# Kernel tuning notes

Measured on AMD Instinct MI355X. Metric: run time of the kernel, lower is better.

The kernel has to match this reference:

```python
import jax, jax.numpy as jnp
import numpy as np

DIM = 768
H = 12        # query heads
HKV = 4       # kv heads
G = H // HKV  # GQA group size
HD = 64       # head dim
CAP = 50.0    # soft cap (Gemma-2 style)
EPS = 1e-6
SCALE = HD ** -0.5
B, T, S = 1, 128, 256


def setup_inputs() -> dict:
    key = jax.random.key(0)
    ks = jax.random.split(key, 5)
    s = DIM ** -0.5
    x = jax.random.normal(ks[0], (B, T, S, DIM), jnp.float32)
    Wq = jax.random.normal(ks[1], (DIM, H * HD), jnp.float32) * s
    Wk = jax.random.normal(ks[2], (DIM, HKV * HD), jnp.float32) * s
    Wv = jax.random.normal(ks[3], (DIM, HKV * HD), jnp.float32) * s
    Wo = jax.random.normal(ks[4], (H * HD, DIM), jnp.float32) * s
    q_norm_w = jnp.ones((HD,), jnp.float32)
    k_norm_w = jnp.ones((HD,), jnp.float32)
    return {"x": x, "Wq": Wq, "Wk": Wk, "Wv": Wv, "Wo": Wo,
            "q_norm_w": q_norm_w, "k_norm_w": k_norm_w}


def _rmsnorm(x, w):
    # x: (..., HD)
    return x * jax.lax.rsqrt(jnp.mean(x * x, axis=-1, keepdims=True) + EPS) * w


def reference(x, Wq, Wk, Wv, Wo, q_norm_w, k_norm_w):
    b, t, s, d = x.shape
    n = b * s
    # fold spatial into batch: temporal attention per spatial position
    xf = x.transpose(0, 2, 1, 3).reshape(n, t, d)             # (N, T, D)
    q = (xf @ Wq).reshape(n, t, H, HD).transpose(0, 2, 1, 3)   # (N, H, T, hd)
    k = (xf @ Wk).reshape(n, t, HKV, HD).transpose(0, 2, 1, 3) # (N, Hkv, T, hd)
    v = (xf @ Wv).reshape(n, t, HKV, HD).transpose(0, 2, 1, 3)
    # QKNorm (per-head RMSNorm on head_dim)
    q = _rmsnorm(q, q_norm_w)
    k = _rmsnorm(k, k_norm_w)
    # GQA without materializing repeated K/V: split q heads into (Hkv, G)
    # (repeat_interleave maps query head h -> kv head h // G, matching kv*G+g)
    qg = q.reshape(n, HKV, G, t, HD)
    attn = jnp.einsum('bkgtd,bksd->bkgts', qg, k) * SCALE      # (N, Hkv, G, T, T)
    attn = CAP * jnp.tanh(attn / CAP)                          # soft cap
    causal = jnp.triu(jnp.ones((t, t), bool), 1)               # True above diag
    attn = jnp.where(causal, -jnp.inf, attn)
    attn = jax.nn.softmax(attn, axis=-1)
    out = jnp.einsum('bkgts,bksd->bkgtd', attn, v)             # (N, Hkv, G, T, hd)
    out = out.reshape(n, H, t, HD).transpose(0, 2, 1, 3).reshape(n, t, H * HD)
    out = out @ Wo                                             # (N, T, D)
    return out.reshape(b, s, t, d).transpose(0, 2, 1, 3)        # (B, T, S, D)
```

## Files before the change

### kernel.cpp

```cpp
#include <hip/hip_runtime.h>
#include <stdint.h>
#include <stddef.h>

#define DIM 768
#define NH  12
#define NKV 4
#define HD  64
#define TT  128
#define NS  256

typedef __attribute__((ext_vector_type(8))) short bf16x8;
typedef __attribute__((ext_vector_type(4))) float f32x4;
typedef __attribute__((ext_vector_type(4))) unsigned int u32x4;
typedef __attribute__((ext_vector_type(2))) unsigned int u32x2;

__device__ __forceinline__ unsigned short f2bf(float f) {
  union { float f; unsigned int u; } v; v.f = f;
  return (unsigned short)((v.u + 0x7FFFu + ((v.u >> 16) & 1u)) >> 16);
}

__global__ __launch_bounds__(256)
void prep_kernel(const float* __restrict__ x, const float* __restrict__ Wq,
                 const float* __restrict__ Wk, const float* __restrict__ Wv,
                 const float* __restrict__ Wo, unsigned short* __restrict__ Wt,
                 unsigned short* __restrict__ WoT, unsigned short* __restrict__ xb) {
  const int b = blockIdx.x, tid = threadIdx.x;
  if (b < 6144) {
    int idx = b * 256 + tid;
    const int n1 = 1280 * DIM;
    if (idx < n1) {
      int c = idx / DIM, kk = idx - c * DIM;
      float v;
      if (c < 768)       v = Wq[kk * 768 + c];
      else if (c < 1024) v = Wk[kk * 256 + (c - 768)];
      else               v = Wv[kk * 256 + (c - 1024)];
      Wt[idx] = f2bf(v);
    } else {
      int i2 = idx - n1;
      int c = i2 / DIM, kk = i2 - c * DIM;
      WoT[i2] = f2bf(Wo[kk * 768 + c]);
    }
  } else {
    int g = (b - 6144) * 256 + tid;
    int r = g / 192;
    int k = g - r * 192;
    int t = r >> 8, n = r & 255;
    f32x4 f = *reinterpret_cast<const f32x4*>(x + (size_t)g * 4);
    u32x2 pk;
    pk[0] = (unsigned)f2bf(f[0]) | ((unsigned)f2bf(f[1]) << 16);
    pk[1] = (unsigned)f2bf(f[2]) | ((unsigned)f2bf(f[3]) << 16);
    *reinterpret_cast<u32x2*>(xb + (size_t)((n << 7) + t) * DIM + k * 4) = pk;
  }
}

__global__ __launch_bounds__(256)
void qkv_kernel(const unsigned short* __restrict__ xb, const float* __restrict__ qnw,
                const float* __restrict__ knw, const unsigned short* __restrict__ Wt,
                unsigned short* __restrict__ qb, unsigned short* __restrict__ kb,
                unsigned short* __restrict__ vTb) {
  const int b = blockIdx.x;
  const int x8 = b & 7, ib = b >> 3;
  const int cb = ib % 10;
  const int n  = (ib / 10) * 8 + x8;
  const int tid = threadIdx.x;
  const int wave = tid >> 6, lane = tid & 63;
  const int cl = lane & 15, rowg = lane >> 4;
  const int wr = wave >> 1, wc = wave & 1;
  __shared__ unsigned short As[128][72];
  __shared__ unsigned short Bs[128][72];
  f32x4 acc[4][4] = {};
  const int col0 = cb * 128;
  for (int ko = 0; ko < DIM; ko += 64) {
    __syncthreads();
    #pragma unroll
    for (int i2 = 0; i2 < 4; ++i2) {
      int c = tid + 256 * i2, r = c >> 3, seg = c & 7;
      *reinterpret_cast<u32x4*>(&As[r][seg * 8]) =
          *reinterpret_cast<const u32x4*>(xb + (size_t)(n * TT + r) * DIM + ko + seg * 8);
    }
    #pragma unroll
    for (int i2 = 0; i2 < 4; ++i2) {
      int c = tid + 256 * i2, r = c >> 3, seg = c & 7;
      *reinterpret_cast<u32x4*>(&Bs[r][seg * 8]) =
          *reinterpret_cast<const u32x4*>(Wt + (size_t)(col0 + r) * DIM + ko + seg * 8);
    }
    __syncthreads();
    #pragma unroll
    for (int ks = 0; ks < 2; ++ks) {
      bf16x8 a[4], bb[4];
      #pragma unroll
      for (int m = 0; m < 4; ++m)
        a[m] = *reinterpret_cast<const bf16x8*>(&As[wr * 64 + m * 16 + cl][ks * 32 + rowg * 8]);
      #pragma unroll
      for (int nn = 0; nn < 4; ++nn)
        bb[nn] = *reinterpret_cast<const bf16x8*>(&Bs[wc * 64 + nn * 16 + cl][ks * 32 + rowg * 8]);
      #pragma unroll
      for (int m = 0; m < 4; ++m)
        #pragma unroll
        for (int nn = 0; nn < 4; ++nn)
          acc[m][nn] = __builtin_amdgcn_mfma_f32_16x16x32_bf16(a[m], bb[nn], acc[m][nn], 0, 0, 0);
    }
  }
  const int typ = (cb < 6) ? 0 : (cb < 8 ? 1 : 2);
  if (typ == 2) {
    const int kv = (cb - 8) * 2 + wc;
    unsigned short* dst = vTb + (size_t)((n * NKV + kv) * HD) * TT;
    #pragma unroll
    for (int m = 0; m < 4; ++m) {
      const int tb = wr * 64 + m * 16 + rowg * 4;
      #pragma unroll
      for (int nn = 0; nn < 4; ++nn) {
        const int d = nn * 16 + cl;
        u32x2 pk;
        pk[0] = (unsigned)f2bf(acc[m][nn][0]) | ((unsigned)f2bf(acc[m][nn][1]) << 16);
        pk[1] = (unsigned)f2bf(acc[m][nn][2]) | ((unsigned)f2bf(acc[m][nn][3]) << 16);
        *reinterpret_cast<u32x2*>(dst + (size_t)d * TT + tb) = pk;
      }
    }
  } else {
    const float* nw = (typ == 0) ? qnw : knw;
    float wfrag[4];
    #pragma unroll
    for (int nn = 0; nn < 4; ++nn) wfrag[nn] = nw[nn * 16 + cl];
    const float rs = (typ == 0) ? 0.125f : 1.0f;
    unsigned short* dst;
    if (typ == 0) { const int hh = cb * 2 + wc; dst = qb + (size_t)(n * NH + hh) * TT * HD; }
    else          { const int kv = (cb - 6) * 2 + wc; dst = kb + (size_t)(n * NKV + kv) * TT * HD; }
    #pragma unroll
    for (int m = 0; m < 4; ++m) {
      #pragma unroll
      for (int j = 0; j < 4; ++j) {
        const int t = wr * 64 + m * 16 + rowg * 4 + j;
        float ss = 0.f;
        #pragma unroll
        for (int nn = 0; nn < 4; ++nn) { float v = acc[m][nn][j]; ss += v * v; }
        #pragma unroll
        for (int dlt = 1; dlt < 16; dlt <<= 1) ss += __shfl_xor(ss, dlt);
        const float r = rsqrtf(ss * (1.f / 64.f) + 1e-6f) * rs;
        #pragma unroll
        for (int nn = 0; nn < 4; ++nn)
          dst[(size_t)t * HD + nn * 16 + cl] = f2bf(acc[m][nn][j] * r * wfrag[nn]);
      }
    }
  }
}

__global__ __launch_bounds__(256)
void attn_kernel(const unsigned short* __restrict__ qb, const unsigned short* __restrict__ kb,
                 const unsigned short* __restrict__ vTb, unsigned short* __restrict__ ab) {
  const int b = blockIdx.x;
  const int x8 = b & 7, ib = b >> 3;
  const int h = ib % 12;
  const int n = (ib / 12) * 8 + x8;
  const int kv = h / 3;
  const int tid = threadIdx.x, wave = tid >> 6, lane = tid & 63;
  const int cl = lane & 15, rowg = lane >> 4;
  __shared__ __align__(16) char smem[52224];
  unsigned short (*Qs)[72]  = reinterpret_cast<unsigned short (*)[72]>(smem);
  unsigned short (*Ks)[72]  = reinterpret_cast<unsigned short (*)[72]>(smem + 18432);
  unsigned short (*Pl)[136] = reinterpret_cast<unsigned short (*)[136]>(smem);
  unsigned short (*Vts)[136] = reinterpret_cast<unsigned short (*)[136]>(smem + 34816);

  const unsigned short* qsrc = qb + (size_t)(n * NH + h) * TT * HD;
  const unsigned short* ksrc = kb + (size_t)(n * NKV + kv) * TT * HD;
  #pragma unroll
  for (int i = 0; i < 4; ++i) {
    int c = tid + 256 * i, r = c >> 3, seg = c & 7;
    *reinterpret_cast<u32x4*>(&Qs[r][seg * 8]) = *reinterpret_cast<const u32x4*>(qsrc + c * 8);
  }
  #pragma unroll
  for (int i = 0; i < 4; ++i) {
    int c = tid + 256 * i, r = c >> 3, seg = c & 7;
    *reinterpret_cast<u32x4*>(&Ks[r][seg * 8]) = *reinterpret_cast<const u32x4*>(ksrc + c * 8);
  }
  __syncthreads();
  f32x4 sc[2][8] = {};
  #pragma unroll
  for (int ks = 0; ks < 2; ++ks) {
    bf16x8 a[2], bbf[8];
    #pragma unroll
    for (int m = 0; m < 2; ++m)
      a[m] = *reinterpret_cast<const bf16x8*>(&Qs[wave * 32 + m * 16 + cl][ks * 32 + rowg * 8]);
    #pragma unroll
    for (int nn = 0; nn < 8; ++nn)
      bbf[nn] = *reinterpret_cast<const bf16x8*>(&Ks[nn * 16 + cl][ks * 32 + rowg * 8]);
    #pragma unroll
    for (int m = 0; m < 2; ++m)
      #pragma unroll
      for (int nn = 0; nn < 8; ++nn)
        sc[m][nn] = __builtin_amdgcn_mfma_f32_16x16x32_bf16(a[m], bbf[nn], sc[m][nn], 0, 0, 0);
  }
  __syncthreads();
  const unsigned short* vsrc = vTb + (size_t)(n * NKV + kv) * HD * TT;
  #pragma unroll
  for (int i = 0; i < 4; ++i) {
    int c = tid + 256 * i, r = c >> 4, seg = c & 15;
    *reinterpret_cast<u32x4*>(&Vts[r][seg * 8]) = *reinterpret_cast<const u32x4*>(vsrc + c * 8);
  }
  #pragma unroll
  for (int m = 0; m < 2; ++m) {
    #pragma unroll
    for (int j = 0; j < 4; ++j) {
      const int rowv = wave * 32 + m * 16 + rowg * 4 + j;
      float mx = -__builtin_inff();
      #pragma unroll
      for (int nn = 0; nn < 8; ++nn) {
        float s = sc[m][nn][j];
        float e = __expf(s * 0.04f);
        s = 50.f - 100.f * __builtin_amdgcn_rcpf(e + 1.f);
        if (nn * 16 + cl > rowv) s = -__builtin_inff();
        sc[m][nn][j] = s;
        mx = fmaxf(mx, s);
      }
      #pragma unroll
      for (int d = 1; d < 16; d <<= 1) mx = fmaxf(mx, __shfl_xor(mx, d));
      float sum = 0.f;
      #pragma unroll
      for (int nn = 0; nn < 8; ++nn) {
        float e = __expf(sc[m][nn][j] - mx);
        sc[m][nn][j] = e;
        sum += e;
      }
      #pragma unroll
      for (int d = 1; d < 16; d <<= 1) sum += __shfl_xor(sum, d);
      const float inv = __builtin_amdgcn_rcpf(sum);
      #pragma unroll
      for (int nn = 0; nn < 8; ++nn)
        Pl[rowv][nn * 16 + cl] = f2bf(sc[m][nn][j] * inv);
    }
  }
  __syncthreads();
  f32x4 o[2][4] = {};
  #pragma unroll
  for (int ks = 0; ks < 4; ++ks) {
    bf16x8 a[2], bbf[4];
    #pragma unroll
    for (int m = 0; m < 2; ++m)
      a[m] = *reinterpret_cast<const bf16x8*>(&Pl[wave * 32 + m * 16 + cl][ks * 32 + rowg * 8]);
    #pragma unroll
    for (int nn = 0; nn < 4; ++nn)
      bbf[nn] = *reinterpret_cast<const bf16x8*>(&Vts[nn * 16 + cl][ks * 32 + rowg * 8]);
    #pragma unroll
    for (int m = 0; m < 2; ++m)
      #pragma unroll
      for (int nn = 0; nn < 4; ++nn)
        o[m][nn] = __builtin_amdgcn_mfma_f32_16x16x32_bf16(a[m], bbf[nn], o[m][nn], 0, 0, 0);
  }
  unsigned short* dst = ab + (size_t)n * TT * 768 + h * 64;
  #pragma unroll
  for (int m = 0; m < 2; ++m)
    #pragma unroll
    for (int j = 0; j < 4; ++j) {
      int t = wave * 32 + m * 16 + rowg * 4 + j;
      #pragma unroll
      for (int nn = 0; nn < 4; ++nn)
        dst[(size_t)t * 768 + nn * 16 + cl] = f2bf(o[m][nn][j]);
    }
}

__global__ __launch_bounds__(256)
void out_kernel(const unsigned short* __restrict__ ab, const unsigned short* __restrict__ WoT,
                float* __restrict__ out) {
  const int b = blockIdx.x;
  const int x8 = b & 7, ib = b >> 3;
  const int cb = ib % 6;
  const int n  = (ib / 6) * 8 + x8;
  const int tid = threadIdx.x, wave = tid >> 6, lane = tid & 63;
  const int cl = lane & 15, rowg = lane >> 4;
  const int wr = wave >> 1, wc = wave & 1;
  __shared__ unsigned short As[128][72];
  __shared__ unsigned short Bs[128][72];
  f32x4 acc[4][4] = {};
  for (int ko = 0; ko < DIM; ko += 64) {
    __syncthreads();
    #pragma unroll
    for (int i2 = 0; i2 < 4; ++i2) {
      int c = tid + 256 * i2, r = c >> 3, seg = c & 7;
      *reinterpret_cast<u32x4*>(&As[r][seg * 8]) =
          *reinterpret_cast<const u32x4*>(ab + (size_t)(n * TT + r) * DIM + ko + seg * 8);
    }
    #pragma unroll
    for (int i2 = 0; i2 < 4; ++i2) {
      int c = tid + 256 * i2, r = c >> 3, seg = c & 7;
      *reinterpret_cast<u32x4*>(&Bs[r][seg * 8]) =
          *reinterpret_cast<const u32x4*>(WoT + (size_t)(cb * 128 + r) * DIM + ko + seg * 8);
    }
    __syncthreads();
    #pragma unroll
    for (int ks = 0; ks < 2; ++ks) {
      bf16x8 a[4], bb[4];
      #pragma unroll
      for (int m = 0; m < 4; ++m)
        a[m] = *reinterpret_cast<const bf16x8*>(&As[wr * 64 + m * 16 + cl][ks * 32 + rowg * 8]);
      #pragma unroll
      for (int nn = 0; nn < 4; ++nn)
        bb[nn] = *reinterpret_cast<const bf16x8*>(&Bs[wc * 64 + nn * 16 + cl][ks * 32 + rowg * 8]);
      #pragma unroll
      for (int m = 0; m < 4; ++m)
        #pragma unroll
        for (int nn = 0; nn < 4; ++nn)
          acc[m][nn] = __builtin_amdgcn_mfma_f32_16x16x32_bf16(a[m], bb[nn], acc[m][nn], 0, 0, 0);
    }
  }
  #pragma unroll
  for (int m = 0; m < 4; ++m)
    #pragma unroll
    for (int j = 0; j < 4; ++j) {
      int t = wr * 64 + m * 16 + rowg * 4 + j;
      #pragma unroll
      for (int nn = 0; nn < 4; ++nn)
        out[(size_t)(t * NS + n) * DIM + cb * 128 + wc * 64 + nn * 16 + cl] = acc[m][nn][j];
    }
}

extern "C" void kernel_launch(void* const* d_in, const int* in_sizes, int n_in,
                              void* d_out, int out_size, void* d_ws, size_t ws_size,
                              hipStream_t stream) {
  const float* x   = (const float*)d_in[0];
  const float* Wq  = (const float*)d_in[1];
  const float* Wk  = (const float*)d_in[2];
  const float* Wv  = (const float*)d_in[3];
  const float* Wo  = (const float*)d_in[4];
  const float* qnw = (const float*)d_in[5];
  const float* knw = (const float*)d_in[6];
  (void)in_sizes; (void)n_in; (void)out_size;

  char* ws = (char*)d_ws;
  unsigned short* Wt  = (unsigned short*)(ws + 0);
  unsigned short* WoT = (unsigned short*)(ws + 1966080);
  unsigned short* qb  = (unsigned short*)(ws + 3145728);
  unsigned short* kb  = (unsigned short*)(ws + 53477376);
  unsigned short* vTb = (unsigned short*)(ws + 70254592);
  unsigned short* ab  = (unsigned short*)(ws + 87031808);
  unsigned short* xb  = ab;
  if (ws_size < 137363456) return;

  prep_kernel<<<30720, 256, 0, stream>>>(x, Wq, Wk, Wv, Wo, Wt, WoT, xb);
  qkv_kernel<<<2560, 256, 0, stream>>>(xb, qnw, knw, Wt, qb, kb, vTb);
  attn_kernel<<<3072, 256, 0, stream>>>(qb, kb, vTb, ab);
  out_kernel<<<1536, 256, 0, stream>>>(ab, WoT, (float*)d_out);
}
```

Before: 239.9 us.

## Double-buffer GEMMs with direct global-to-LDS loads and share K/V across GQA heads

The QKV and output GEMMs move to 512-thread blocks with 128x256 tiles. Tiles are double-buffered in dynamic LDS and filled with global_load_lds using an XOR swizzle, so the next K-tile loads while MFMAs run on the current one. The attention kernel now processes all three query heads of a KV group in one block, loading K and V^T into LDS once and reading Q straight from global memory. The trade is larger LDS use and lower occupancy against less redundant K/V traffic and better load/compute overlap.

```diff
diff --git a/kernel.cpp b/kernel.cpp
--- a/kernel.cpp
+++ b/kernel.cpp
@@ -17,6 +17,12 @@
 __device__ __forceinline__ unsigned short f2bf(float f) {
   union { float f; unsigned int u; } v; v.f = f;
   return (unsigned short)((v.u + 0x7FFFu + ((v.u >> 16) & 1u)) >> 16);
+}
+
+__device__ __forceinline__ void gload_lds16(const void* g, void* l) {
+  __builtin_amdgcn_global_load_lds(
+      (const __attribute__((address_space(1))) unsigned int*)g,
+      (__attribute__((address_space(3))) unsigned int*)l, 16, 0, 0);
 }
 
 __global__ __launch_bounds__(256)
@@ -53,61 +59,73 @@
   }
 }
 
-__global__ __launch_bounds__(256)
+__global__ __launch_bounds__(512, 2)
 void qkv_kernel(const unsigned short* __restrict__ xb, const float* __restrict__ qnw,
                 const float* __restrict__ knw, const unsigned short* __restrict__ Wt,
                 unsigned short* __restrict__ qb, unsigned short* __restrict__ kb,
                 unsigned short* __restrict__ vTb) {
+  extern __shared__ unsigned short lds[];
   const int b = blockIdx.x;
-  const int x8 = b & 7, ib = b >> 3;
-  const int cb = ib % 10;
-  const int n  = (ib / 10) * 8 + x8;
+  const int x8 = b & 7, idx = b >> 3;
+  const int cbt = idx % 5;
+  const int n   = (idx / 5) * 8 + x8;
   const int tid = threadIdx.x;
   const int wave = tid >> 6, lane = tid & 63;
   const int cl = lane & 15, rowg = lane >> 4;
-  const int wr = wave >> 1, wc = wave & 1;
-  __shared__ unsigned short As[128][72];
-  __shared__ unsigned short Bs[128][72];
+  const int wmw = wave >> 2, wn = wave & 3;
+  const int l8 = lane >> 3, s8 = lane & 7;
+  const int col0 = cbt * 256;
+  const unsigned short* asrc = xb + (size_t)(n * TT + l8) * DIM + (s8 ^ l8) * 8;
+  const unsigned short* bsrc = Wt + (size_t)(col0 + l8) * DIM + (s8 ^ l8) * 8;
+  const int swzr = (cl & 7) << 4;
   f32x4 acc[4][4] = {};
-  const int col0 = cb * 128;
-  for (int ko = 0; ko < DIM; ko += 64) {
-    __syncthreads();
-    #pragma unroll
-    for (int i2 = 0; i2 < 4; ++i2) {
-      int c = tid + 256 * i2, r = c >> 3, seg = c & 7;
-      *reinterpret_cast<u32x4*>(&As[r][seg * 8]) =
-          *reinterpret_cast<const u32x4*>(xb + (size_t)(n * TT + r) * DIM + ko + seg * 8);
-    }
-    #pragma unroll
-    for (int i2 = 0; i2 < 4; ++i2) {
-      int c = tid + 256 * i2, r = c >> 3, seg = c & 7;
-      *reinterpret_cast<u32x4*>(&Bs[r][seg * 8]) =
-          *reinterpret_cast<const u32x4*>(Wt + (size_t)(col0 + r) * DIM + ko + seg * 8);
-    }
-    __syncthreads();
+
+#define QKV_STAGE(buf, ko)                                                  \
+  {                                                                         \
+    unsigned short* Ad = lds + (buf) * 24576;                               \
+    unsigned short* Bd = Ad + 8192;                                         \
+    _Pragma("unroll")                                                       \
+    for (int i = 0; i < 2; ++i) {                                           \
+      const int r0 = i * 64 + wave * 8;                                     \
+      gload_lds16(asrc + (size_t)r0 * DIM + (ko), Ad + r0 * 64);            \
+    }                                                                       \
+    _Pragma("unroll")                                                       \
+    for (int i = 0; i < 4; ++i) {                                           \
+      const int r0 = i * 64 + wave * 8;                                     \
+      gload_lds16(bsrc + (size_t)r0 * DIM + (ko), Bd + r0 * 64);            \
+    }                                                                       \
+  }
+
+  QKV_STAGE(0, 0);
+  __syncthreads();
+  for (int kt = 0; kt < 12; ++kt) {
+    if (kt < 11) QKV_STAGE((kt + 1) & 1, (kt + 1) * 64);
+    const char* Ab = (const char*)(lds + (kt & 1) * 24576);
+    const char* Bb = Ab + 16384;
     #pragma unroll
     for (int ks = 0; ks < 2; ++ks) {
       bf16x8 a[4], bb[4];
       #pragma unroll
       for (int m = 0; m < 4; ++m)
-        a[m] = *reinterpret_cast<const bf16x8*>(&As[wr * 64 + m * 16 + cl][ks * 32 + rowg * 8]);
+        a[m] = *(const bf16x8*)(Ab + (wmw * 64 + m * 16 + cl) * 128 + ((ks * 64 + rowg * 16) ^ swzr));
       #pragma unroll
       for (int nn = 0; nn < 4; ++nn)
-        bb[nn] = *reinterpret_cast<const bf16x8*>(&Bs[wc * 64 + nn * 16 + cl][ks * 32 + rowg * 8]);
+        bb[nn] = *(const bf16x8*)(Bb + (wn * 64 + nn * 16 + cl) * 128 + ((ks * 64 + rowg * 16) ^ swzr));
       #pragma unroll
       for (int m = 0; m < 4; ++m)
         #pragma unroll
         for (int nn = 0; nn < 4; ++nn)
           acc[m][nn] = __builtin_amdgcn_mfma_f32_16x16x32_bf16(a[m], bb[nn], acc[m][nn], 0, 0, 0);
     }
-  }
-  const int typ = (cb < 6) ? 0 : (cb < 8 ? 1 : 2);
-  if (typ == 2) {
-    const int kv = (cb - 8) * 2 + wc;
+    __syncthreads();
+  }
+
+  if (cbt == 4) {
+    const int kv = wn;
     unsigned short* dst = vTb + (size_t)((n * NKV + kv) * HD) * TT;
     #pragma unroll
     for (int m = 0; m < 4; ++m) {
-      const int tb = wr * 64 + m * 16 + rowg * 4;
+      const int tb = wmw * 64 + m * 16 + rowg * 4;
       #pragma unroll
       for (int nn = 0; nn < 4; ++nn) {
         const int d = nn * 16 + cl;
@@ -118,19 +136,20 @@
       }
     }
   } else {
-    const float* nw = (typ == 0) ? qnw : knw;
+    const int isq = (cbt < 3);
+    const float* nw = isq ? qnw : knw;
     float wfrag[4];
     #pragma unroll
     for (int nn = 0; nn < 4; ++nn) wfrag[nn] = nw[nn * 16 + cl];
-    const float rs = (typ == 0) ? 0.125f : 1.0f;
+    const float rs = isq ? 0.125f : 1.0f;
     unsigned short* dst;
-    if (typ == 0) { const int hh = cb * 2 + wc; dst = qb + (size_t)(n * NH + hh) * TT * HD; }
-    else          { const int kv = (cb - 6) * 2 + wc; dst = kb + (size_t)(n * NKV + kv) * TT * HD; }
+    if (isq) { const int hh = cbt * 4 + wn; dst = qb + (size_t)(n * NH + hh) * TT * HD; }
+    else     { const int kv = wn;           dst = kb + (size_t)(n * NKV + kv) * TT * HD; }
     #pragma unroll
     for (int m = 0; m < 4; ++m) {
       #pragma unroll
       for (int j = 0; j < 4; ++j) {
-        const int t = wr * 64 + m * 16 + rowg * 4 + j;
+        const int t = wmw * 64 + m * 16 + rowg * 4 + j;
         float ss = 0.f;
         #pragma unroll
         for (int nn = 0; nn < 4; ++nn) { float v = acc[m][nn][j]; ss += v * v; }
@@ -143,174 +162,187 @@
       }
     }
   }
+#undef QKV_STAGE
 }
 
 __global__ __launch_bounds__(256)
 void attn_kernel(const unsigned short* __restrict__ qb, const unsigned short* __restrict__ kb,
                  const unsigned short* __restrict__ vTb, unsigned short* __restrict__ ab) {
+  extern __shared__ char smem[];
+  unsigned short (*Ks)[72]   = reinterpret_cast<unsigned short (*)[72]>(smem);
+  unsigned short (*Vts)[136] = reinterpret_cast<unsigned short (*)[136]>(smem + 18432);
+  unsigned short (*Pl)[136]  = reinterpret_cast<unsigned short (*)[136]>(smem + 35840);
   const int b = blockIdx.x;
-  const int x8 = b & 7, ib = b >> 3;
-  const int h = ib % 12;
-  const int n = (ib / 12) * 8 + x8;
-  const int kv = h / 3;
+  const int x8 = b & 7, idx = b >> 3;
+  const int kv = idx & 3;
+  const int n  = (idx >> 2) * 8 + x8;
   const int tid = threadIdx.x, wave = tid >> 6, lane = tid & 63;
   const int cl = lane & 15, rowg = lane >> 4;
-  __shared__ __align__(16) char smem[52224];
-  unsigned short (*Qs)[72]  = reinterpret_cast<unsigned short (*)[72]>(smem);
-  unsigned short (*Ks)[72]  = reinterpret_cast<unsigned short (*)[72]>(smem + 18432);
-  unsigned short (*Pl)[136] = reinterpret_cast<unsigned short (*)[136]>(smem);
-  unsigned short (*Vts)[136] = reinterpret_cast<unsigned short (*)[136]>(smem + 34816);
-
-  const unsigned short* qsrc = qb + (size_t)(n * NH + h) * TT * HD;
+
   const unsigned short* ksrc = kb + (size_t)(n * NKV + kv) * TT * HD;
-  #pragma unroll
-  for (int i = 0; i < 4; ++i) {
-    int c = tid + 256 * i, r = c >> 3, seg = c & 7;
-    *reinterpret_cast<u32x4*>(&Qs[r][seg * 8]) = *reinterpret_cast<const u32x4*>(qsrc + c * 8);
-  }
+  const unsigned short* vsrc = vTb + (size_t)(n * NKV + kv) * HD * TT;
   #pragma unroll
   for (int i = 0; i < 4; ++i) {
     int c = tid + 256 * i, r = c >> 3, seg = c & 7;
     *reinterpret_cast<u32x4*>(&Ks[r][seg * 8]) = *reinterpret_cast<const u32x4*>(ksrc + c * 8);
   }
-  __syncthreads();
-  f32x4 sc[2][8] = {};
-  #pragma unroll
-  for (int ks = 0; ks < 2; ++ks) {
-    bf16x8 a[2], bbf[8];
-    #pragma unroll
-    for (int m = 0; m < 2; ++m)
-      a[m] = *reinterpret_cast<const bf16x8*>(&Qs[wave * 32 + m * 16 + cl][ks * 32 + rowg * 8]);
-    #pragma unroll
-    for (int nn = 0; nn < 8; ++nn)
-      bbf[nn] = *reinterpret_cast<const bf16x8*>(&Ks[nn * 16 + cl][ks * 32 + rowg * 8]);
-    #pragma unroll
-    for (int m = 0; m < 2; ++m)
-      #pragma unroll
-      for (int nn = 0; nn < 8; ++nn)
-        sc[m][nn] = __builtin_amdgcn_mfma_f32_16x16x32_bf16(a[m], bbf[nn], sc[m][nn], 0, 0, 0);
-  }
-  __syncthreads();
-  const unsigned short* vsrc = vTb + (size_t)(n * NKV + kv) * HD * TT;
   #pragma unroll
   for (int i = 0; i < 4; ++i) {
     int c = tid + 256 * i, r = c >> 4, seg = c & 15;
     *reinterpret_cast<u32x4*>(&Vts[r][seg * 8]) = *reinterpret_cast<const u32x4*>(vsrc + c * 8);
   }
-  #pragma unroll
-  for (int m = 0; m < 2; ++m) {
-    #pragma unroll
-    for (int j = 0; j < 4; ++j) {
-      const int rowv = wave * 32 + m * 16 + rowg * 4 + j;
-      float mx = -__builtin_inff();
-      #pragma unroll
-      for (int nn = 0; nn < 8; ++nn) {
-        float s = sc[m][nn][j];
-        float e = __expf(s * 0.04f);
-        s = 50.f - 100.f * __builtin_amdgcn_rcpf(e + 1.f);
-        if (nn * 16 + cl > rowv) s = -__builtin_inff();
-        sc[m][nn][j] = s;
-        mx = fmaxf(mx, s);
+  __syncthreads();
+
+  for (int hh = 0; hh < 3; ++hh) {
+    const int h = kv * 3 + hh;
+    const unsigned short* qsrc = qb + (size_t)(n * NH + h) * TT * HD;
+    f32x4 sc[2][8] = {};
+    #pragma unroll
+    for (int ks = 0; ks < 2; ++ks) {
+      bf16x8 a[2], bbf[8];
+      #pragma unroll
+      for (int m = 0; m < 2; ++m)
+        a[m] = *reinterpret_cast<const bf16x8*>(
+            qsrc + (size_t)(wave * 32 + m * 16 + cl) * HD + ks * 32 + rowg * 8);
+      #pragma unroll
+      for (int nn = 0; nn < 8; ++nn)
+        bbf[nn] = *reinterpret_cast<const bf16x8*>(&Ks[nn * 16 + cl][ks * 32 + rowg * 8]);
+      #pragma unroll
+      for (int m = 0; m < 2; ++m)
+        #pragma unroll
+        for (int nn = 0; nn < 8; ++nn)
+          sc[m][nn] = __builtin_amdgcn_mfma_f32_16x16x32_bf16(a[m], bbf[nn], sc[m][nn], 0, 0, 0);
+    }
+    #pragma unroll
+    for (int m = 0; m < 2; ++m) {
+      #pragma unroll
+      for (int j = 0; j < 4; ++j) {
+        const int rowv = wave * 32 + m * 16 + rowg * 4 + j;
+        float mx = -__builtin_inff();
+        #pragma unroll
+        for (int nn = 0; nn < 8; ++nn) {
+          float s = sc[m][nn][j];
+          float e = __expf(s * 0.04f);
+          s = 50.f - 100.f * __builtin_amdgcn_rcpf(e + 1.f);
+          if (nn * 16 + cl > rowv) s = -__builtin_inff();
+          sc[m][nn][j] = s;
+          mx = fmaxf(mx, s);
+        }
+        #pragma unroll
+        for (int d = 1; d < 16; d <<= 1) mx = fmaxf(mx, __shfl_xor(mx, d));
+        float sum = 0.f;
+        #pragma unroll
+        for (int nn = 0; nn < 8; ++nn) {
+          float e = __expf(sc[m][nn][j] - mx);
+          sc[m][nn][j] = e;
+          sum += e;
+        }
+        #pragma unroll
+        for (int d = 1; d < 16; d <<= 1) sum += __shfl_xor(sum, d);
+        const float inv = __builtin_amdgcn_rcpf(sum);
+        #pragma unroll
+        for (int nn = 0; nn < 8; ++nn)
+          Pl[rowv][nn * 16 + cl] = f2bf(sc[m][nn][j] * inv);
       }
-      #pragma unroll
-      for (int d = 1; d < 16; d <<= 1) mx = fmaxf(mx, __shfl_xor(mx, d));
-      float sum = 0.f;
-      #pragma unroll
-      for (int nn = 0; nn < 8; ++nn) {
-        float e = __expf(sc[m][nn][j] - mx);
-        sc[m][nn][j] = e;
-        sum += e;
+    }
+    __syncthreads();
+    f32x4 o[2][4] = {};
+    #pragma unroll
+    for (int ks = 0; ks < 4; ++ks) {
+      bf16x8 a[2], bbf[4];
+      #pragma unroll
+      for (int m = 0; m < 2; ++m)
+        a[m] = *reinterpret_cast<const bf16x8*>(&Pl[wave * 32 + m * 16 + cl][ks * 32 + rowg * 8]);
+      #pragma unroll
+      for (int nn = 0; nn < 4; ++nn)
+        bbf[nn] = *reinterpret_cast<const bf16x8*>(&Vts[nn * 16 + cl][ks * 32 + rowg * 8]);
+      #pragma unroll
+      for (int m = 0; m < 2; ++m)
+        #pragma unroll
+        for (int nn = 0; nn < 4; ++nn)
+          o[m][nn] = __builtin_amdgcn_mfma_f32_16x16x32_bf16(a[m], bbf[nn], o[m][nn], 0, 0, 0);
+    }
+    unsigned short* dst = ab + (size_t)n * TT * DIM + h * HD;
+    #pragma unroll
+    for (int m = 0; m < 2; ++m)
+      #pragma unroll
+      for (int j = 0; j < 4; ++j) {
+        int t = wave * 32 + m * 16 + rowg * 4 + j;
+        #pragma unroll
+        for (int nn = 0; nn < 4; ++nn)
+          dst[(size_t)t * DIM + nn * 16 + cl] = f2bf(o[m][nn][j]);
       }
-      #pragma unroll
-      for (int d = 1; d < 16; d <<= 1) sum += __shfl_xor(sum, d);
-      const float inv = __builtin_amdgcn_rcpf(sum);
-      #pragma unroll
-      for (int nn = 0; nn < 8; ++nn)
-        Pl[rowv][nn * 16 + cl] = f2bf(sc[m][nn][j] * inv);
-    }
-  }
-  __syncthreads();
-  f32x4 o[2][4] = {};
-  #pragma unroll
-  for (int ks = 0; ks < 4; ++ks) {
-    bf16x8 a[2], bbf[4];
-    #pragma unroll
-    for (int m = 0; m < 2; ++m)
-      a[m] = *reinterpret_cast<const bf16x8*>(&Pl[wave * 32 + m * 16 + cl][ks * 32 + rowg * 8]);
-    #pragma unroll
-    for (int nn = 0; nn < 4; ++nn)
-      bbf[nn] = *reinterpret_cast<const bf16x8*>(&Vts[nn * 16 + cl][ks * 32 + rowg * 8]);
-    #pragma unroll
-    for (int m = 0; m < 2; ++m)
-      #pragma unroll
-      for (int nn = 0; nn < 4; ++nn)
-        o[m][nn] = __builtin_amdgcn_mfma_f32_16x16x32_bf16(a[m], bbf[nn], o[m][nn], 0, 0, 0);
-  }
-  unsigned short* dst = ab + (size_t)n * TT * 768 + h * 64;
-  #pragma unroll
-  for (int m = 0; m < 2; ++m)
-    #pragma unroll
-    for (int j = 0; j < 4; ++j) {
-      int t = wave * 32 + m * 16 + rowg * 4 + j;
-      #pragma unroll
-      for (int nn = 0; nn < 4; ++nn)
-        dst[(size_t)t * 768 + nn * 16 + cl] = f2bf(o[m][nn][j]);
-    }
-}
-
-__global__ __launch_bounds__(256)
+    __syncthreads();
+  }
+}
+
+__global__ __launch_bounds__(512, 2)
 void out_kernel(const unsigned short* __restrict__ ab, const unsigned short* __restrict__ WoT,
                 float* __restrict__ out) {
+  extern __shared__ unsigned short lds[];
   const int b = blockIdx.x;
-  const int x8 = b & 7, ib = b >> 3;
-  const int cb = ib % 6;
-  const int n  = (ib / 6) * 8 + x8;
-  const int tid = threadIdx.x, wave = tid >> 6, lane = tid & 63;
+  const int x8 = b & 7, idx = b >> 3;
+  const int cbt = idx % 3;
+  const int n   = (idx / 3) * 8 + x8;
+  const int tid = threadIdx.x;
+  const int wave = tid >> 6, lane = tid & 63;
   const int cl = lane & 15, rowg = lane >> 4;
-  const int wr = wave >> 1, wc = wave & 1;
-  __shared__ unsigned short As[128][72];
-  __shared__ unsigned short Bs[128][72];
+  const int wmw = wave >> 2, wn = wave & 3;
+  const int l8 = lane >> 3, s8 = lane & 7;
+  const unsigned short* asrc = ab  + (size_t)(n * TT + l8) * DIM + (s8 ^ l8) * 8;
+  const unsigned short* bsrc = WoT + (size_t)(cbt * 256 + l8) * DIM + (s8 ^ l8) * 8;
+  const int swzr = (cl & 7) << 4;
   f32x4 acc[4][4] = {};
-  for (int ko = 0; ko < DIM; ko += 64) {
-    __syncthreads();
-    #pragma unroll
-    for (int i2 = 0; i2 < 4; ++i2) {
-      int c = tid + 256 * i2, r = c >> 3, seg = c & 7;
-      *reinterpret_cast<u32x4*>(&As[r][seg * 8]) =
-          *reinterpret_cast<const u32x4*>(ab + (size_t)(n * TT + r) * DIM + ko + seg * 8);
-    }
-    #pragma unroll
-    for (int i2 = 0; i2 < 4; ++i2) {
-      int c = tid + 256 * i2, r = c >> 3, seg = c & 7;
-      *reinterpret_cast<u32x4*>(&Bs[r][seg * 8]) =
-          *reinterpret_cast<const u32x4*>(WoT + (size_t)(cb * 128 + r) * DIM + ko + seg * 8);
-    }
-    __syncthreads();
+
+#define OUT_STAGE(buf, ko)                                                  \
+  {                                                                         \
+    unsigned short* Ad = lds + (buf) * 24576;                               \
+    unsigned short* Bd = Ad + 8192;                                         \
+    _Pragma("unroll")                                                       \
+    for (int i = 0; i < 2; ++i) {                                           \
+      const int r0 = i * 64 + wave * 8;                                     \
+      gload_lds16(asrc + (size_t)r0 * DIM + (ko), Ad + r0 * 64);            \
+    }                                                                       \
+    _Pragma("unroll")                                                       \
+    for (int i = 0; i < 4; ++i) {                                           \
+      const int r0 = i * 64 + wave * 8;                                     \
+      gload_lds16(bsrc + (size_t)r0 * DIM + (ko), Bd + r0 * 64);            \
+    }                                                                       \
+  }
+
+  OUT_STAGE(0, 0);
+  __syncthreads();
+  for (int kt = 0; kt < 12; ++kt) {
+    if (kt < 11) OUT_STAGE((kt + 1) & 1, (kt + 1) * 64);
+    const char* Ab = (const char*)(lds + (kt & 1) * 24576);
+    const char* Bb = Ab + 16384;
     #pragma unroll
     for (int ks = 0; ks < 2; ++ks) {
       bf16x8 a[4], bb[4];
       #pragma unroll
       for (int m = 0; m < 4; ++m)
-        a[m] = *reinterpret_cast<const bf16x8*>(&As[wr * 64 + m * 16 + cl][ks * 32 + rowg * 8]);
+        a[m] = *(const bf16x8*)(Ab + (wmw * 64 + m * 16 + cl) * 128 + ((ks * 64 + rowg * 16) ^ swzr));
       #pragma unroll
       for (int nn = 0; nn < 4; ++nn)
-        bb[nn] = *reinterpret_cast<const bf16x8*>(&Bs[wc * 64 + nn * 16 + cl][ks * 32 + rowg * 8]);
+        bb[nn] = *(const bf16x8*)(Bb + (wn * 64 + nn * 16 + cl) * 128 + ((ks * 64 + rowg * 16) ^ swzr));
       #pragma unroll
       for (int m = 0; m < 4; ++m)
         #pragma unroll
         for (int nn = 0; nn < 4; ++nn)
           acc[m][nn] = __builtin_amdgcn_mfma_f32_16x16x32_bf16(a[m], bb[nn], acc[m][nn], 0, 0, 0);
     }
+    __syncthreads();
   }
   #pragma unroll
   for (int m = 0; m < 4; ++m)
     #pragma unroll
     for (int j = 0; j < 4; ++j) {
-      int t = wr * 64 + m * 16 + rowg * 4 + j;
+      int t = wmw * 64 + m * 16 + rowg * 4 + j;
       #pragma unroll
       for (int nn = 0; nn < 4; ++nn)
-        out[(size_t)(t * NS + n) * DIM + cb * 128 + wc * 64 + nn * 16 + cl] = acc[m][nn][j];
-    }
+        out[(size_t)(t * NS + n) * DIM + cbt * 256 + wn * 64 + nn * 16 + cl] = acc[m][nn][j];
+    }
+#undef OUT_STAGE
 }
 
 extern "C" void kernel_launch(void* const* d_in, const int* in_sizes, int n_in,
@@ -335,8 +367,15 @@
   unsigned short* xb  = ab;
   if (ws_size < 137363456) return;
 
+  hipFuncSetAttribute(reinterpret_cast<const void*>(qkv_kernel),
+                      hipFuncAttributeMaxDynamicSharedMemorySize, 98304);
+  hipFuncSetAttribute(reinterpret_cast<const void*>(out_kernel),
+                      hipFuncAttributeMaxDynamicSharedMemorySize, 98304);
+  hipFuncSetAttribute(reinterpret_cast<const void*>(attn_kernel),
+                      hipFuncAttributeMaxDynamicSharedMemorySize, 70656);
+
   prep_kernel<<<30720, 256, 0, stream>>>(x, Wq, Wk, Wv, Wo, Wt, WoT, xb);
-  qkv_kernel<<<2560, 256, 0, stream>>>(xb, qnw, knw, Wt, qb, kb, vTb);
-  attn_kernel<<<3072, 256, 0, stream>>>(qb, kb, vTb, ab);
-  out_kernel<<<1536, 256, 0, stream>>>(ab, WoT, (float*)d_out);
-}
+  qkv_kernel<<<1280, 512, 98304, stream>>>(xb, qnw, knw, Wt, qb, kb, vTb);
+  attn_kernel<<<1024, 256, 70656, stream>>>(qb, kb, vTb, ab);
+  out_kernel<<<768, 512, 98304, stream>>>(ab, WoT, (float*)d_out);
+}
```

Result: faster. 219.5 us (-8.5%).
